# Performance work log

Hardware: AMD Instinct MI355X
Metric: run time of the kernel (lower is better)

Reference implementation:

```python
import jax, jax.numpy as jnp
import numpy as np

HID, HEADS, FF, DEPTH = 1152, 16, 4304, 2
HD = HID // HEADS            # 72
ROT = HD // 2                # 36 (rotary_pos_emb width)
S, NSEG = 2048, 4
EPS = 1e-6


def _layernorm(x, w, b):
    m = jnp.mean(x, axis=-1, keepdims=True)
    xc = x - m
    v = jnp.mean(xc * xc, axis=-1, keepdims=True)
    return xc * jax.lax.rsqrt(v + EPS) * w + b


def _rotate_half(x):
    x1, x2 = jnp.split(x, 2, axis=-1)
    return jnp.concatenate([-x2, x1], axis=-1)


def _apply_rotary(t, freqs):
    # t: [S, H, D], freqs: [S, D/2]
    emb = jnp.concatenate([freqs, freqs], axis=-1)          # [S, D]
    cos = jnp.cos(emb)[:, None, :]
    sin = jnp.sin(emb)[:, None, :]
    return t * cos + _rotate_half(t) * sin


def setup_inputs() -> dict:
    key = jax.random.key(0)
    ks = jax.random.split(key, 16)
    sd = 0.02
    # rotary freqs as in VisionRotaryEmbedding(dim=HD//2): h-pos and w-pos halves
    inv_freq = 1.0 / (10000.0 ** (jnp.arange(0, ROT, 2, dtype=jnp.float32) / ROT))  # [18]
    pos = jnp.arange(S, dtype=jnp.float32)
    hpos, wpos = pos // 32.0, pos % 32.0
    rotary = jnp.concatenate([jnp.outer(hpos, inv_freq), jnp.outer(wpos, inv_freq)], axis=-1)  # [S, 36]
    return {
        "x": jax.random.normal(ks[0], (S, HID), jnp.float32),
        "cu_seqlens": jnp.arange(NSEG + 1, dtype=jnp.int32) * (S // NSEG),
        "rotary_pos_emb": rotary,
        "norm1_w": jnp.ones((DEPTH, HID), jnp.float32),
        "norm1_b": jnp.zeros((DEPTH, HID), jnp.float32),
        "qkv_w": jax.random.normal(ks[1], (DEPTH, 3 * HID, HID), jnp.float32) * sd,
        "qkv_b": jnp.zeros((DEPTH, 3 * HID), jnp.float32),
        "proj_w": jax.random.normal(ks[2], (DEPTH, HID, HID), jnp.float32) * sd,
        "proj_b": jnp.zeros((DEPTH, HID), jnp.float32),
        "norm2_w": jnp.ones((DEPTH, HID), jnp.float32),
        "norm2_b": jnp.zeros((DEPTH, HID), jnp.float32),
        "fc1_w": jax.random.normal(ks[3], (DEPTH, FF, HID), jnp.float32) * sd,
        "fc1_b": jnp.zeros((DEPTH, FF), jnp.float32),
        "fc2_w": jax.random.normal(ks[4], (DEPTH, HID, FF), jnp.float32) * sd,
        "fc2_b": jnp.zeros((DEPTH, HID), jnp.float32),
    }


def _forward(x, cu_seqlens, rotary_pos_emb, norm1_w, norm1_b, qkv_w, qkv_b,
             proj_w, proj_b, norm2_w, norm2_b, fc1_w, fc1_b, fc2_w, fc2_b):
    seq_len = x.shape[0]
    # block-diagonal additive mask from cu_seqlens (same mask the torch loop builds)
    seg = jnp.searchsorted(cu_seqlens, jnp.arange(seq_len, dtype=cu_seqlens.dtype), side="right") - 1
    same = seg[:, None] == seg[None, :]
    bias = jnp.where(same, jnp.float32(0.0), jnp.finfo(jnp.float32).min)  # [S, S]
    scale = 1.0 / np.sqrt(HD)
    for d in range(DEPTH):
        # --- attention ---
        h = _layernorm(x, norm1_w[d], norm1_b[d])
        qkv = (h @ qkv_w[d].T + qkv_b[d]).reshape(seq_len, 3, HEADS, HD)
        q, k, v = qkv[:, 0], qkv[:, 1], qkv[:, 2]           # [S, H, D]
        q = _apply_rotary(q, rotary_pos_emb)
        k = _apply_rotary(k, rotary_pos_emb)
        scores = jnp.einsum("qhd,khd->hqk", q, k) * scale + bias[None]
        probs = jax.nn.softmax(scores.astype(jnp.float32), axis=-1).astype(q.dtype)
        attn = jnp.einsum("hqk,khd->qhd", probs, v).reshape(seq_len, HID)
        x = x + attn @ proj_w[d].T + proj_b[d]
        # --- MLP (gelu tanh approx) ---
        h2 = _layernorm(x, norm2_w[d], norm2_b[d])
        x = x + jax.nn.gelu(h2 @ fc1_w[d].T + fc1_b[d], approximate=True) @ fc2_w[d].T + fc2_b[d]
    return x


def reference(x, cu_seqlens, rotary_pos_emb, norm1_w, norm1_b, qkv_w, qkv_b,
              proj_w, proj_b, norm2_w, norm2_b, fc1_w, fc1_b, fc2_w, fc2_b):
    return _forward(x, cu_seqlens, rotary_pos_emb, norm1_w, norm1_b, qkv_w, qkv_b,
                    proj_w, proj_b, norm2_w, norm2_b, fc1_w, fc1_b, fc2_w, fc2_b)
```

## Files before the change

kernel.cpp:

```cpp
#include <hip/hip_runtime.h>

#define S_LEN 2048
#define HID   1152
#define HEADS 16
#define HD    72
#define ROT   36
#define LD3   3456
#define FF    4304
#define FFP   4320

typedef short s16x8 __attribute__((ext_vector_type(8)));
typedef short s16x4 __attribute__((ext_vector_type(4)));
typedef float f32x4 __attribute__((ext_vector_type(4)));
typedef short bf_t;

__device__ __forceinline__ short f2b(float f) {
  unsigned u = __float_as_uint(f);
  u += 0x7fffu + ((u >> 16) & 1u);
  return (short)(u >> 16);
}
__device__ __forceinline__ float b2f(short h) {
  return __uint_as_float(((unsigned)(unsigned short)h) << 16);
}
__device__ __forceinline__ float gelu_f(float x) {
  float t = tanhf(0.7978845608028654f * (x + 0.044715f * x * x * x));
  return 0.5f * x * (1.0f + t);
}

typedef const __attribute__((address_space(1))) void* gas_p;
typedef __attribute__((address_space(3))) void* las_p;
__device__ __forceinline__ void gload16(const void* g, void* l) {
  __builtin_amdgcn_global_load_lds((gas_p)g, (las_p)l, 16, 0, 0);
}

__global__ __launch_bounds__(256) void convw4_kernel(
    const float* __restrict__ src, int N, int K,
    bf_t* __restrict__ dst, int Kpad)
{
  int idx = blockIdx.x * 256 + threadIdx.x;
  int kq = Kpad >> 2;
  if (idx >= N * kq) return;
  int n = idx / kq, k = (idx % kq) << 2;
  s16x4 o;
  if (k + 3 < K) {
    float4 v = *(const float4*)(src + (size_t)n * K + k);
    o[0] = f2b(v.x); o[1] = f2b(v.y); o[2] = f2b(v.z); o[3] = f2b(v.w);
  } else {
#pragma unroll
    for (int j = 0; j < 4; j++) {
      int kk = k + j;
      o[j] = (kk < K) ? f2b(src[(size_t)n * K + kk]) : (short)0;
    }
  }
  *(s16x4*)(dst + (size_t)n * Kpad + k) = o;
}

__global__ __launch_bounds__(256) void costab_kernel(
    const float* __restrict__ rot, float* __restrict__ ct, float* __restrict__ st)
{
  int i = blockIdx.x * 256 + threadIdx.x;
  if (i < S_LEN * ROT) { float f = rot[i]; ct[i] = cosf(f); st[i] = sinf(f); }
}

__global__ __launch_bounds__(256) void ln_kernel(
    const float* __restrict__ x, const float* __restrict__ wgt,
    const float* __restrict__ bia, bf_t* __restrict__ outb)
{
  const int row = blockIdx.x, tid = threadIdx.x;
  const float4* xr = (const float4*)(x + (size_t)row * HID);
  float4 a = xr[tid];
  float4 b2 = make_float4(0.f, 0.f, 0.f, 0.f);
  const bool has2 = tid < 32;
  if (has2) b2 = xr[256 + tid];
  float s = a.x + a.y + a.z + a.w + b2.x + b2.y + b2.z + b2.w;
  float q = a.x*a.x + a.y*a.y + a.z*a.z + a.w*a.w
          + b2.x*b2.x + b2.y*b2.y + b2.z*b2.z + b2.w*b2.w;
  for (int mk = 32; mk; mk >>= 1) { s += __shfl_xor(s, mk); q += __shfl_xor(q, mk); }
  __shared__ float red[16];
  if ((tid & 63) == 0) { red[tid >> 6] = s; red[8 + (tid >> 6)] = q; }
  __syncthreads();
  if (tid == 0) {
    red[4]  = red[0] + red[1] + red[2] + red[3];
    red[12] = red[8] + red[9] + red[10] + red[11];
  }
  __syncthreads();
  float mean = red[4] * (1.0f / HID);
  float var  = red[12] * (1.0f / HID) - mean * mean;
  float rstd = rsqrtf(var + 1e-6f);
  const float4* w4 = (const float4*)wgt;
  const float4* b4 = (const float4*)bia;
  s16x4* o4 = (s16x4*)(outb + (size_t)row * HID);
  {
    float4 wv = w4[tid], bv = b4[tid];
    s16x4 o;
    o[0] = f2b((a.x - mean) * rstd * wv.x + bv.x);
    o[1] = f2b((a.y - mean) * rstd * wv.y + bv.y);
    o[2] = f2b((a.z - mean) * rstd * wv.z + bv.z);
    o[3] = f2b((a.w - mean) * rstd * wv.w + bv.w);
    o4[tid] = o;
  }
  if (has2) {
    float4 wv = w4[256 + tid], bv = b4[256 + tid];
    s16x4 o;
    o[0] = f2b((b2.x - mean) * rstd * wv.x + bv.x);
    o[1] = f2b((b2.y - mean) * rstd * wv.y + bv.y);
    o[2] = f2b((b2.z - mean) * rstd * wv.z + bv.z);
    o[3] = f2b((b2.w - mean) * rstd * wv.w + bv.w);
    o4[256 + tid] = o;
  }
}

__global__ __launch_bounds__(256) void rotary_kernel(
    bf_t* __restrict__ qkv, const float* __restrict__ ct, const float* __restrict__ st)
{
  int idx = blockIdx.x * 256 + threadIdx.x;
  if (idx >= S_LEN * HEADS * ROT) return;
  int t = idx / (HEADS * ROT);
  int r = idx % (HEADS * ROT);
  int h = r / ROT, dd = r % ROT;
  float c = ct[t * ROT + dd], s = st[t * ROT + dd];
  size_t base = (size_t)t * LD3 + h * HD + dd;
  float q1 = b2f(qkv[base]),        q2 = b2f(qkv[base + ROT]);
  float k1 = b2f(qkv[base + HID]),  k2 = b2f(qkv[base + HID + ROT]);
  const float scale = 0.11785113019775793f;
  qkv[base]             = f2b((q1 * c - q2 * s) * scale);
  qkv[base + ROT]       = f2b((q2 * c + q1 * s) * scale);
  qkv[base + HID]       = f2b(k1 * c - k2 * s);
  qkv[base + HID + ROT] = f2b(k2 * c + k1 * s);
}

template<int MODE>
__global__ __launch_bounds__(256, 4) void gemm1(
    const bf_t* __restrict__ A, int lda,
    const bf_t* __restrict__ B, int ldb,
    const float* __restrict__ bias, int nbias,
    void* outp, int ldc, int nvalid, int K, int kchunk)
{
  __shared__ __align__(16) bf_t As[128 * 32];
  __shared__ __align__(16) bf_t Bs[128 * 32];
  const int tid = threadIdx.x;
  const int l = tid & 63, w = tid >> 6;
  const int lr = l & 15, lg = l >> 4;
  const int wm = (w >> 1) * 64, wn = (w & 1) * 64;

  unsigned gx = gridDim.x, gy = gridDim.y, gz = gridDim.z;
  unsigned nwg = gx * gy * gz;
  unsigned lin = (blockIdx.z * gy + blockIdx.y) * gx + blockIdx.x;
  if ((nwg & 7u) == 0u) {
    unsigned q = nwg >> 3;
    lin = (lin & 7u) * q + (lin >> 3);
  }
  const unsigned bz = lin / (gx * gy);
  const unsigned rem = lin % (gx * gy);
  const unsigned by = rem / gx, bx = rem % gx;

  const int rowA0 = by * 128, colB0 = bx * 128;
  const int kb0 = bz * kchunk;
  int kb1 = kb0 + kchunk; if (kb1 > K) kb1 = K;

  const int o1 = tid * 16, o2 = o1 + 4096;
  const int r1 = o1 >> 6, c1 = o1 & 63;
  const int r2 = o2 >> 6, c2 = o2 & 63;
  const char* Ab = (const char*)A;
  const char* Bb = (const char*)B;

  f32x4 acc[4][4] = {};

  for (int kb = kb0; kb < kb1; kb += 32) {
    gload16(Ab + ((size_t)(rowA0 + r1) * lda + kb) * 2 + c1, (char*)As + o1);
    gload16(Ab + ((size_t)(rowA0 + r2) * lda + kb) * 2 + c2, (char*)As + o2);
    gload16(Bb + ((size_t)(colB0 + r1) * ldb + kb) * 2 + c1, (char*)Bs + o1);
    gload16(Bb + ((size_t)(colB0 + r2) * ldb + kb) * 2 + c2, (char*)Bs + o2);
    asm volatile("s_waitcnt vmcnt(0)" ::: "memory");
    __syncthreads();
    s16x8 af[4], bv[4];
#pragma unroll
    for (int mt = 0; mt < 4; mt++) af[mt] = *(const s16x8*)&As[(wm + mt * 16 + lr) * 32 + lg * 8];
#pragma unroll
    for (int nt = 0; nt < 4; nt++) bv[nt] = *(const s16x8*)&Bs[(wn + nt * 16 + lr) * 32 + lg * 8];
#pragma unroll
    for (int mt = 0; mt < 4; mt++)
#pragma unroll
      for (int nt = 0; nt < 4; nt++)
        acc[mt][nt] = __builtin_amdgcn_mfma_f32_16x16x32_bf16(af[mt], bv[nt], acc[mt][nt], 0, 0, 0);
    __syncthreads();
  }

#pragma unroll
  for (int mt = 0; mt < 4; mt++) {
    const int rr = rowA0 + wm + mt * 16 + lg * 4;
#pragma unroll
    for (int nt = 0; nt < 4; nt++) {
      const int cc = colB0 + wn + nt * 16 + lr;
      const float bvl = (cc < nbias) ? bias[cc] : 0.0f;
#pragma unroll
      for (int i = 0; i < 4; i++) {
        float v = acc[mt][nt][i] + bvl;
        const int row = rr + i;
        if (MODE == 0) {
          ((bf_t*)outp)[(size_t)row * ldc + cc] = f2b(v);
        } else if (MODE == 2) {
          if (cc < nvalid)      ((bf_t*)outp)[(size_t)row * ldc + cc] = f2b(gelu_f(v));
          else if (cc < ldc)    ((bf_t*)outp)[(size_t)row * ldc + cc] = 0;
        } else {
          float* P = (float*)outp + (size_t)bz * ((size_t)S_LEN * ldc);
          P[(size_t)row * ldc + cc] = v;
        }
      }
    }
  }
}

template<int MODE>
__global__ __launch_bounds__(256, 4) void gemm2(
    const bf_t* __restrict__ A, int lda,
    const bf_t* __restrict__ B, int ldb,
    const float* __restrict__ bias, int nbias,
    void* outp, int ldc, int nvalid, int K, int kchunk)
{
  __shared__ __align__(16) bf_t As[2][128 * 32];
  __shared__ __align__(16) bf_t Bs[2][64 * 32];
  const int tid = threadIdx.x;
  const int l = tid & 63, w = tid >> 6;
  const int lr = l & 15, lg = l >> 4;
  const int wm = (w >> 1) * 64, wn = (w & 1) * 32;

  unsigned gx = gridDim.x, gy = gridDim.y, gz = gridDim.z;
  unsigned nwg = gx * gy * gz;
  unsigned lin = (blockIdx.z * gy + blockIdx.y) * gx + blockIdx.x;
  if ((nwg & 7u) == 0u) {
    unsigned q = nwg >> 3;
    lin = (lin & 7u) * q + (lin >> 3);
  }
  const unsigned bz = lin / (gx * gy);
  const unsigned rem = lin % (gx * gy);
  const unsigned by = rem / gx, bx = rem % gx;

  const int rowA0 = by * 128, colB0 = bx * 64;
  const int kb0 = bz * kchunk;
  int kb1 = kb0 + kchunk; if (kb1 > K) kb1 = K;

  const int oA1 = tid * 16, oA2 = oA1 + 4096;
  const int rA1 = oA1 >> 6, cA1 = oA1 & 63;
  const int rA2 = rA1 + 64;
  const int oB = tid * 16;
  const int rB = oB >> 6, cB = oB & 63;
  const char* Ab = (const char*)A;
  const char* Bb = (const char*)B;

#define STAGE(buf, kk) do { \
    gload16(Ab + ((size_t)(rowA0 + rA1) * lda + (kk)) * 2 + cA1, (char*)As[buf] + oA1); \
    gload16(Ab + ((size_t)(rowA0 + rA2) * lda + (kk)) * 2 + cA1, (char*)As[buf] + oA2); \
    gload16(Bb + ((size_t)(colB0 + rB)  * ldb + (kk)) * 2 + cB,  (char*)Bs[buf] + oB);  \
  } while (0)

  f32x4 acc[4][2] = {};

  STAGE(0, kb0);
  asm volatile("s_waitcnt vmcnt(0)" ::: "memory");
  __builtin_amdgcn_s_barrier();
  __builtin_amdgcn_sched_barrier(0);

  int cur = 0;
  for (int kb = kb0; kb < kb1; kb += 32) {
    if (kb + 32 < kb1) STAGE(cur ^ 1, kb + 32);
    s16x8 af[4], bv[2];
#pragma unroll
    for (int mt = 0; mt < 4; mt++)
      af[mt] = *(const s16x8*)&As[cur][(wm + mt * 16 + lr) * 32 + lg * 8];
#pragma unroll
    for (int nt = 0; nt < 2; nt++)
      bv[nt] = *(const s16x8*)&Bs[cur][(wn + nt * 16 + lr) * 32 + lg * 8];
    asm volatile("s_waitcnt lgkmcnt(0)" ::: "memory");
    __builtin_amdgcn_sched_barrier(0);
#pragma unroll
    for (int mt = 0; mt < 4; mt++)
#pragma unroll
      for (int nt = 0; nt < 2; nt++)
        acc[mt][nt] = __builtin_amdgcn_mfma_f32_16x16x32_bf16(af[mt], bv[nt], acc[mt][nt], 0, 0, 0);
    asm volatile("s_waitcnt vmcnt(0)" ::: "memory");
    __builtin_amdgcn_s_barrier();
    __builtin_amdgcn_sched_barrier(0);
    cur ^= 1;
  }
#undef STAGE

#pragma unroll
  for (int mt = 0; mt < 4; mt++) {
    const int rr = rowA0 + wm + mt * 16 + lg * 4;
#pragma unroll
    for (int nt = 0; nt < 2; nt++) {
      const int cc = colB0 + wn + nt * 16 + lr;
      const float bvl = (cc < nbias) ? bias[cc] : 0.0f;
#pragma unroll
      for (int i = 0; i < 4; i++) {
        float v = acc[mt][nt][i] + bvl;
        const int row = rr + i;
        if (MODE == 0) {
          ((bf_t*)outp)[(size_t)row * ldc + cc] = f2b(v);
        } else if (MODE == 2) {
          if (cc < nvalid)      ((bf_t*)outp)[(size_t)row * ldc + cc] = f2b(gelu_f(v));
          else if (cc < ldc)    ((bf_t*)outp)[(size_t)row * ldc + cc] = 0;
        } else {
          float* P = (float*)outp + (size_t)bz * ((size_t)S_LEN * ldc);
          P[(size_t)row * ldc + cc] = v;
        }
      }
    }
  }
}

__global__ __launch_bounds__(256) void reduce_kernel(
    const float* __restrict__ part, const float* __restrict__ bias,
    const float* __restrict__ resid, float* __restrict__ outp)
{
  int idx = blockIdx.x * 256 + threadIdx.x;
  if (idx >= S_LEN * HID / 4) return;
  float4 r = ((const float4*)resid)[idx];
  float4 bv = ((const float4*)bias)[idx % (HID / 4)];
  float sx = r.x + bv.x, sy = r.y + bv.y, sz = r.z + bv.z, sw = r.w + bv.w;
#pragma unroll
  for (int p = 0; p < 4; p++) {
    float4 v = ((const float4*)(part + (size_t)p * S_LEN * HID))[idx];
    sx += v.x; sy += v.y; sz += v.z; sw += v.w;
  }
  ((float4*)outp)[idx] = make_float4(sx, sy, sz, sw);
}

#define QSTR 104
#define VSTR 72
#define PSTR 72
__global__ __launch_bounds__(256, 2) void attn_kernel(
    const bf_t* __restrict__ qkv, const int* __restrict__ cu, int nseg,
    bf_t* __restrict__ outb)
{
  __shared__ __align__(16) bf_t Qs[64 * QSTR];
  __shared__ __align__(16) bf_t Ks[64 * QSTR];
  __shared__ __align__(16) bf_t VTs[80 * VSTR];
  __shared__ __align__(16) bf_t Pb[4][16 * PSTR];
  const int tid = threadIdx.x;
  const int l = tid & 63, w = tid >> 6;
  const int lr = l & 15, lg = l >> 4;
  const int h = blockIdx.y;
  const int qbase = blockIdx.x * 64;

  int kstart = 0, kend = S_LEN;
  for (int s2 = 0; s2 < nseg; s2++) {
    int a = cu[s2], b = cu[s2 + 1];
    if (qbase >= a && qbase < b) { kstart = a; kend = b; }
  }

  for (int i = tid; i < 64 * QSTR; i += 256)
    if ((i % QSTR) >= HD) { Qs[i] = 0; Ks[i] = 0; }
  for (int i = tid; i < 80 * VSTR; i += 256)
    if ((i / VSTR) >= HD) VTs[i] = 0;
  for (int c = tid; c < 576; c += 256) {
    int r = c / 9, j = c % 9;
    *(s16x8*)&Qs[r * QSTR + j * 8] =
        *(const s16x8*)&qkv[(size_t)(qbase + r) * LD3 + h * HD + j * 8];
  }
  __syncthreads();
  s16x8 qf[3];
#pragma unroll
  for (int ks = 0; ks < 3; ks++)
    qf[ks] = *(const s16x8*)&Qs[(w * 16 + lr) * QSTR + ks * 32 + lg * 8];

  float m_i[4], l_i[4];
  f32x4 Of[5] = {};
#pragma unroll
  for (int i = 0; i < 4; i++) { m_i[i] = -1e30f; l_i[i] = 0.0f; }

  for (int kb = kstart; kb < kend; kb += 64) {
    __syncthreads();
    for (int c = tid; c < 576; c += 256) {
      int r = c / 9, j = c % 9;
      int gr = kb + r; if (gr >= kend) gr = kend - 1;
      *(s16x8*)&Ks[r * QSTR + j * 8] =
          *(const s16x8*)&qkv[(size_t)gr * LD3 + HID + h * HD + j * 8];
    }
    for (int c = tid; c < 576; c += 256) {
      int r = c / 9, j = c % 9;
      int gr = kb + r; if (gr >= kend) gr = kend - 1;
      s16x8 v = *(const s16x8*)&qkv[(size_t)gr * LD3 + 2 * HID + h * HD + j * 8];
#pragma unroll
      for (int jj = 0; jj < 8; jj++) VTs[(j * 8 + jj) * VSTR + r] = v[jj];
    }
    __syncthreads();

    f32x4 sc[4] = {};
#pragma unroll
    for (int kc = 0; kc < 4; kc++) {
#pragma unroll
      for (int ks = 0; ks < 3; ks++) {
        s16x8 kf = *(const s16x8*)&Ks[(kc * 16 + lr) * QSTR + ks * 32 + lg * 8];
        sc[kc] = __builtin_amdgcn_mfma_f32_16x16x32_bf16(qf[ks], kf, sc[kc], 0, 0, 0);
      }
    }
#pragma unroll
    for (int kc = 0; kc < 4; kc++) {
      if ((kb + kc * 16 + lr) >= kend) {
#pragma unroll
        for (int i = 0; i < 4; i++) sc[kc][i] = -1e30f;
      }
    }
    float tmax[4], scl[4], rs[4];
#pragma unroll
    for (int i = 0; i < 4; i++) {
      float t = fmaxf(fmaxf(sc[0][i], sc[1][i]), fmaxf(sc[2][i], sc[3][i]));
#pragma unroll
      for (int d2 = 1; d2 < 16; d2 <<= 1) t = fmaxf(t, __shfl_xor(t, d2));
      tmax[i] = t;
    }
#pragma unroll
    for (int i = 0; i < 4; i++) {
      float mn = fmaxf(m_i[i], tmax[i]);
      scl[i] = __expf(m_i[i] - mn);
      m_i[i] = mn;
      rs[i] = 0.0f;
    }
#pragma unroll
    for (int kc = 0; kc < 4; kc++)
#pragma unroll
      for (int i = 0; i < 4; i++) {
        float p = __expf(sc[kc][i] - m_i[i]);
        sc[kc][i] = p;
        rs[i] += p;
      }
#pragma unroll
    for (int i = 0; i < 4; i++) {
#pragma unroll
      for (int d2 = 1; d2 < 16; d2 <<= 1) rs[i] += __shfl_xor(rs[i], d2);
      l_i[i] = l_i[i] * scl[i] + rs[i];
    }
#pragma unroll
    for (int nt = 0; nt < 5; nt++)
#pragma unroll
      for (int i = 0; i < 4; i++) Of[nt][i] *= scl[i];
#pragma unroll
    for (int kc = 0; kc < 4; kc++)
#pragma unroll
      for (int i = 0; i < 4; i++)
        Pb[w][(lg * 4 + i) * PSTR + kc * 16 + lr] = f2b(sc[kc][i]);
    __syncthreads();
    s16x8 pf[2];
#pragma unroll
    for (int k2 = 0; k2 < 2; k2++)
      pf[k2] = *(const s16x8*)&Pb[w][lr * PSTR + k2 * 32 + lg * 8];
#pragma unroll
    for (int nt = 0; nt < 5; nt++) {
#pragma unroll
      for (int k2 = 0; k2 < 2; k2++) {
        s16x8 vf = *(const s16x8*)&VTs[(nt * 16 + lr) * VSTR + k2 * 32 + lg * 8];
        Of[nt] = __builtin_amdgcn_mfma_f32_16x16x32_bf16(pf[k2], vf, Of[nt], 0, 0, 0);
      }
    }
  }
  float inv[4];
#pragma unroll
  for (int i = 0; i < 4; i++) inv[i] = 1.0f / l_i[i];
#pragma unroll
  for (int nt = 0; nt < 5; nt++) {
    int cc = nt * 16 + lr;
    if (cc < HD) {
#pragma unroll
      for (int i = 0; i < 4; i++) {
        int row = qbase + w * 16 + lg * 4 + i;
        outb[(size_t)row * HID + h * HD + cc] = f2b(Of[nt][i] * inv[i]);
      }
    }
  }
}

extern "C" void kernel_launch(void* const* d_in, const int* in_sizes, int n_in,
                              void* d_out, int out_size, void* d_ws, size_t ws_size,
                              hipStream_t stream) {
  const float* x     = (const float*)d_in[0];
  const int*   cu    = (const int*)d_in[1];
  const float* rotab = (const float*)d_in[2];
  const float* n1w   = (const float*)d_in[3];
  const float* n1b   = (const float*)d_in[4];
  const float* qkvw  = (const float*)d_in[5];
  const float* qkvb  = (const float*)d_in[6];
  const float* projw = (const float*)d_in[7];
  const float* projb = (const float*)d_in[8];
  const float* n2w   = (const float*)d_in[9];
  const float* n2b   = (const float*)d_in[10];
  const float* fc1w  = (const float*)d_in[11];
  const float* fc1b  = (const float*)d_in[12];
  const float* fc2w  = (const float*)d_in[13];
  const float* fc2b  = (const float*)d_in[14];
  float* out = (float*)d_out;
  char* ws = (char*)d_ws;

  size_t off = 0;
  float* xbuf = (float*)(ws + off); off += (size_t)S_LEN * HID * 4;
  bf_t* hbf   = (bf_t*)(ws + off);  off += (size_t)S_LEN * HID * 2;
  bf_t* qkvbf = (bf_t*)(ws + off);
  bf_t* ff1bf = (bf_t*)(ws + off);  off += (size_t)S_LEN * FFP * 2;
  bf_t* attnbf= (bf_t*)(ws + off);  off += (size_t)S_LEN * HID * 2;
  bf_t* wslot = (bf_t*)(ws + off);  off += (size_t)4352 * 1152 * 2;
  float* ctab = (float*)(ws + off); off += (size_t)S_LEN * ROT * 4;
  float* stab = (float*)(ws + off); off += (size_t)S_LEN * ROT * 4;
  float* part = (float*)(ws + off); off += (size_t)4 * S_LEN * HID * 4;

  costab_kernel<<<(S_LEN * ROT + 255) / 256, 256, 0, stream>>>(rotab, ctab, stab);

  const int nseg = in_sizes[1] - 1;
  const int RED_GRID = (S_LEN * HID / 4 + 255) / 256;

  for (int d = 0; d < 2; d++) {
    const float* xin = (d == 0) ? x : xbuf;
    ln_kernel<<<S_LEN, 256, 0, stream>>>(xin, n1w + d * HID, n1b + d * HID, hbf);
    convw4_kernel<<<(LD3 * HID / 4 + 255) / 256, 256, 0, stream>>>(
        qkvw + (size_t)d * LD3 * HID, LD3, HID, wslot, HID);
    gemm2<0><<<dim3(LD3 / 64, 16), 256, 0, stream>>>(
        hbf, HID, wslot, HID, qkvb + (size_t)d * LD3, LD3, qkvbf, LD3, LD3, HID, HID);
    rotary_kernel<<<(S_LEN * HEADS * ROT + 255) / 256, 256, 0, stream>>>(qkvbf, ctab, stab);
    attn_kernel<<<dim3(S_LEN / 64, HEADS), 256, 0, stream>>>(qkvbf, cu, nseg, attnbf);
    convw4_kernel<<<(HID * HID / 4 + 255) / 256, 256, 0, stream>>>(
        projw + (size_t)d * HID * HID, HID, HID, wslot, HID);
    gemm1<3><<<dim3(HID / 128, 16, 4), 256, 0, stream>>>(
        attnbf, HID, wslot, HID, nullptr, 0, part, HID, HID, HID, 288);
    reduce_kernel<<<RED_GRID, 256, 0, stream>>>(part, projb + (size_t)d * HID, xin, xbuf);
    ln_kernel<<<S_LEN, 256, 0, stream>>>(xbuf, n2w + d * HID, n2b + d * HID, hbf);
    convw4_kernel<<<(FF * HID / 4 + 255) / 256, 256, 0, stream>>>(
        fc1w + (size_t)d * FF * HID, FF, HID, wslot, HID);
    gemm2<2><<<dim3(4352 / 64, 16), 256, 0, stream>>>(
        hbf, HID, wslot, HID, fc1b + (size_t)d * FF, FF, ff1bf, FFP, FF, HID, HID);
    convw4_kernel<<<(HID * FFP / 4 + 255) / 256, 256, 0, stream>>>(
        fc2w + (size_t)d * HID * FF, HID, FF, wslot, FFP);
    gemm1<3><<<dim3(HID / 128, 16, 4), 256, 0, stream>>>(
        ff1bf, FFP, wslot, FFP, nullptr, 0, part, HID, HID, FFP, 1088);
    float* outp = (d == 1) ? out : xbuf;
    reduce_kernel<<<RED_GRID, 256, 0, stream>>>(part, fc2b + (size_t)d * HID, xbuf, outp);
  }
}
```

Measured before the change: 450.6 us.

## Double-buffer K/V tiles in attention with register prefetch and padded V stride

The attention kernel now double-buffers the K and transposed-V tiles in shared memory and prefetches the next tile into registers while computing on the current one. This removes one block barrier per tile, and the per-wave P buffer now uses a waitcnt instead of a full __syncthreads. The V transpose stride is padded to 76 to reduce bank conflicts, and V fragments are read as two 4-element loads to fit the new alignment. The changes add shared memory and register pressure and may cut occupancy. Smaller tweaks skip the bias load in the MODE 3 GEMM epilogue and size the fc1 grid to the padded width.

```diff
diff --git a/kernel.cpp b/kernel.cpp
--- a/kernel.cpp
+++ b/kernel.cpp
@@ -192,7 +192,7 @@
 #pragma unroll
     for (int nt = 0; nt < 4; nt++) {
       const int cc = colB0 + wn + nt * 16 + lr;
-      const float bvl = (cc < nbias) ? bias[cc] : 0.0f;
+      const float bvl = (MODE == 3) ? 0.0f : ((cc < nbias) ? bias[cc] : 0.0f);
 #pragma unroll
       for (int i = 0; i < 4; i++) {
         float v = acc[mt][nt][i] + bvl;
@@ -328,15 +328,15 @@
 }
 
 #define QSTR 104
-#define VSTR 72
+#define VSTR 76
 #define PSTR 72
 __global__ __launch_bounds__(256, 2) void attn_kernel(
     const bf_t* __restrict__ qkv, const int* __restrict__ cu, int nseg,
     bf_t* __restrict__ outb)
 {
   __shared__ __align__(16) bf_t Qs[64 * QSTR];
-  __shared__ __align__(16) bf_t Ks[64 * QSTR];
-  __shared__ __align__(16) bf_t VTs[80 * VSTR];
+  __shared__ __align__(16) bf_t Ks[2][64 * QSTR];
+  __shared__ __align__(16) bf_t VTs[2][80 * VSTR];
   __shared__ __align__(16) bf_t Pb[4][16 * PSTR];
   const int tid = threadIdx.x;
   const int l = tid & 63, w = tid >> 6;
@@ -351,15 +351,39 @@
   }
 
   for (int i = tid; i < 64 * QSTR; i += 256)
-    if ((i % QSTR) >= HD) { Qs[i] = 0; Ks[i] = 0; }
+    if ((i % QSTR) >= HD) { Qs[i] = 0; Ks[0][i] = 0; Ks[1][i] = 0; }
   for (int i = tid; i < 80 * VSTR; i += 256)
-    if ((i / VSTR) >= HD) VTs[i] = 0;
+    if ((i / VSTR) >= HD) { VTs[0][i] = 0; VTs[1][i] = 0; }
   for (int c = tid; c < 576; c += 256) {
     int r = c / 9, j = c % 9;
     *(s16x8*)&Qs[r * QSTR + j * 8] =
         *(const s16x8*)&qkv[(size_t)(qbase + r) * LD3 + h * HD + j * 8];
   }
+  {
+#pragma unroll
+    for (int u = 0; u < 3; u++) {
+      int c = tid + u * 256;
+      if (c < 576) {
+        int r = c / 9, j = c % 9;
+        int gr = kstart + r; if (gr >= kend) gr = kend - 1;
+        *(s16x8*)&Ks[0][r * QSTR + j * 8] =
+            *(const s16x8*)&qkv[(size_t)gr * LD3 + HID + h * HD + j * 8];
+      }
+    }
+#pragma unroll
+    for (int u = 0; u < 3; u++) {
+      int c = tid + u * 256;
+      if (c < 576) {
+        int r = c & 63, j = c >> 6;
+        int gr = kstart + r; if (gr >= kend) gr = kend - 1;
+        s16x8 v = *(const s16x8*)&qkv[(size_t)gr * LD3 + 2 * HID + h * HD + j * 8];
+#pragma unroll
+        for (int jj = 0; jj < 8; jj++) VTs[0][(j * 8 + jj) * VSTR + r] = v[jj];
+      }
+    }
+  }
   __syncthreads();
+
   s16x8 qf[3];
 #pragma unroll
   for (int ks = 0; ks < 3; ks++)
@@ -370,29 +394,41 @@
 #pragma unroll
   for (int i = 0; i < 4; i++) { m_i[i] = -1e30f; l_i[i] = 0.0f; }
 
-  for (int kb = kstart; kb < kend; kb += 64) {
-    __syncthreads();
-    for (int c = tid; c < 576; c += 256) {
-      int r = c / 9, j = c % 9;
-      int gr = kb + r; if (gr >= kend) gr = kend - 1;
-      *(s16x8*)&Ks[r * QSTR + j * 8] =
-          *(const s16x8*)&qkv[(size_t)gr * LD3 + HID + h * HD + j * 8];
-    }
-    for (int c = tid; c < 576; c += 256) {
-      int r = c / 9, j = c % 9;
-      int gr = kb + r; if (gr >= kend) gr = kend - 1;
-      s16x8 v = *(const s16x8*)&qkv[(size_t)gr * LD3 + 2 * HID + h * HD + j * 8];
-#pragma unroll
-      for (int jj = 0; jj < 8; jj++) VTs[(j * 8 + jj) * VSTR + r] = v[jj];
-    }
-    __syncthreads();
+  const int ntile = (kend - kstart + 63) >> 6;
+  int cur = 0;
+  for (int t = 0; t < ntile; t++) {
+    const int kb = kstart + t * 64;
+    const bool more = (t + 1 < ntile);
+
+    s16x8 kreg[3], vreg[3];
+    if (more) {
+      const int nb = kb + 64;
+#pragma unroll
+      for (int u = 0; u < 3; u++) {
+        int c = tid + u * 256;
+        if (c < 576) {
+          int r = c / 9, j = c % 9;
+          int gr = nb + r; if (gr >= kend) gr = kend - 1;
+          kreg[u] = *(const s16x8*)&qkv[(size_t)gr * LD3 + HID + h * HD + j * 8];
+        }
+      }
+#pragma unroll
+      for (int u = 0; u < 3; u++) {
+        int c = tid + u * 256;
+        if (c < 576) {
+          int r = c & 63, j = c >> 6;
+          int gr = nb + r; if (gr >= kend) gr = kend - 1;
+          vreg[u] = *(const s16x8*)&qkv[(size_t)gr * LD3 + 2 * HID + h * HD + j * 8];
+        }
+      }
+    }
 
     f32x4 sc[4] = {};
 #pragma unroll
     for (int kc = 0; kc < 4; kc++) {
 #pragma unroll
       for (int ks = 0; ks < 3; ks++) {
-        s16x8 kf = *(const s16x8*)&Ks[(kc * 16 + lr) * QSTR + ks * 32 + lg * 8];
+        s16x8 kf = *(const s16x8*)&Ks[cur][(kc * 16 + lr) * QSTR + ks * 32 + lg * 8];
         sc[kc] = __builtin_amdgcn_mfma_f32_16x16x32_bf16(qf[ks], kf, sc[kc], 0, 0, 0);
       }
     }
@@ -406,10 +442,10 @@
     float tmax[4], scl[4], rs[4];
 #pragma unroll
     for (int i = 0; i < 4; i++) {
-      float t = fmaxf(fmaxf(sc[0][i], sc[1][i]), fmaxf(sc[2][i], sc[3][i]));
-#pragma unroll
-      for (int d2 = 1; d2 < 16; d2 <<= 1) t = fmaxf(t, __shfl_xor(t, d2));
-      tmax[i] = t;
+      float tm = fmaxf(fmaxf(sc[0][i], sc[1][i]), fmaxf(sc[2][i], sc[3][i]));
+#pragma unroll
+      for (int d2 = 1; d2 < 16; d2 <<= 1) tm = fmaxf(tm, __shfl_xor(tm, d2));
+      tmax[i] = tm;
     }
 #pragma unroll
     for (int i = 0; i < 4; i++) {
@@ -441,7 +477,8 @@
 #pragma unroll
       for (int i = 0; i < 4; i++)
         Pb[w][(lg * 4 + i) * PSTR + kc * 16 + lr] = f2b(sc[kc][i]);
-    __syncthreads();
+    asm volatile("s_waitcnt lgkmcnt(0)" ::: "memory");
+    __builtin_amdgcn_sched_barrier(0);
     s16x8 pf[2];
 #pragma unroll
     for (int k2 = 0; k2 < 2; k2++)
@@ -450,11 +487,40 @@
     for (int nt = 0; nt < 5; nt++) {
 #pragma unroll
       for (int k2 = 0; k2 < 2; k2++) {
-        s16x8 vf = *(const s16x8*)&VTs[(nt * 16 + lr) * VSTR + k2 * 32 + lg * 8];
+        const int vb = (nt * 16 + lr) * VSTR + k2 * 32 + lg * 8;
+        s16x4 va = *(const s16x4*)&VTs[cur][vb];
+        s16x4 vb2 = *(const s16x4*)&VTs[cur][vb + 4];
+        s16x8 vf;
+        vf[0] = va[0]; vf[1] = va[1]; vf[2] = va[2]; vf[3] = va[3];
+        vf[4] = vb2[0]; vf[5] = vb2[1]; vf[6] = vb2[2]; vf[7] = vb2[3];
         Of[nt] = __builtin_amdgcn_mfma_f32_16x16x32_bf16(pf[k2], vf, Of[nt], 0, 0, 0);
       }
     }
-  }
+
+    if (more) {
+#pragma unroll
+      for (int u = 0; u < 3; u++) {
+        int c = tid + u * 256;
+        if (c < 576) {
+          int r = c / 9, j = c % 9;
+          *(s16x8*)&Ks[cur ^ 1][r * QSTR + j * 8] = kreg[u];
+        }
+      }
+#pragma unroll
+      for (int u = 0; u < 3; u++) {
+        int c = tid + u * 256;
+        if (c < 576) {
+          int r = c & 63, j = c >> 6;
+#pragma unroll
+          for (int jj = 0; jj < 8; jj++)
+            VTs[cur ^ 1][(j * 8 + jj) * VSTR + r] = vreg[u][jj];
+        }
+      }
+    }
+    __syncthreads();
+    cur ^= 1;
+  }
+
   float inv[4];
 #pragma unroll
   for (int i = 0; i < 4; i++) inv[i] = 1.0f / l_i[i];
@@ -525,13 +591,13 @@
     ln_kernel<<<S_LEN, 256, 0, stream>>>(xbuf, n2w + d * HID, n2b + d * HID, hbf);
     convw4_kernel<<<(FF * HID / 4 + 255) / 256, 256, 0, stream>>>(
         fc1w + (size_t)d * FF * HID, FF, HID, wslot, HID);
-    gemm2<2><<<dim3(4352 / 64, 16), 256, 0, stream>>>(
+    gemm2<2><<<dim3((FFP + 63) / 64, 16), 256, 0, stream>>>(
         hbf, HID, wslot, HID, fc1b + (size_t)d * FF, FF, ff1bf, FFP, FF, HID, HID);
     convw4_kernel<<<(HID * FFP / 4 + 255) / 256, 256, 0, stream>>>(
         fc2w + (size_t)d * HID * FF, HID, FF, wslot, FFP);
+    float* outp = (d == 1) ? out : xbuf;
     gemm1<3><<<dim3(HID / 128, 16, 4), 256, 0, stream>>>(
         ff1bf, FFP, wslot, FFP, nullptr, 0, part, HID, HID, FFP, 1088);
-    float* outp = (d == 1) ? out : xbuf;
     reduce_kernel<<<RED_GRID, 256, 0, stream>>>(part, fc2b + (size_t)d * HID, xbuf, outp);
   }
 }
```

Measured after the change: 436.0 us. 3.2% less time.
